# Kernel tuning notes

Measured on AMD Instinct MI355X. Metric: run time of the kernel, lower is better.

Reference implementation:

```python
import jax, jax.numpy as jnp
import numpy as np
import math

HID = 4096
SLOTS = 8
HEADS = 8
BD = 512  # bottleneck_dim
HD = BD // HEADS  # effective head dim = 64
B, S = 4, 4096


def setup_inputs() -> dict:
    key = jax.random.key(0)
    ks = jax.random.split(key, 8)
    std = 1.0 / math.sqrt(HID)
    return {
        "hidden_states": jax.random.normal(ks[0], (B, S, HID), dtype=jnp.float32),
        "attention_mask": jax.random.randint(ks[1], (B, S), 0, 2, dtype=jnp.int32),
        "memory_slots": jax.random.normal(ks[2], (SLOTS, HID), dtype=jnp.float32) * std,
        # torch nn.Linear weights are [out_features, in_features]
        "Wq": jax.random.normal(ks[3], (BD, HID), dtype=jnp.float32) * std,
        "Wk": jax.random.normal(ks[4], (BD, HID), dtype=jnp.float32) * std,
        "Wv": jax.random.normal(ks[5], (BD, HID), dtype=jnp.float32) * std,
        "Wo": jax.random.normal(ks[6], (HID, BD), dtype=jnp.float32) * (1.0 / math.sqrt(BD)),
    }


def reference(hidden_states, attention_mask, memory_slots, Wq, Wk, Wv, Wo):
    # Q from learnable slots (same for every batch element): [slots, BD]
    Q = memory_slots @ Wq.T
    Q = Q.reshape(SLOTS, HEADS, HD)                      # n h d
    # K/V from sequence: [b, s, BD] -> [b, s, h, d]
    K = jnp.einsum('bsi,oi->bso', hidden_states, Wk).reshape(B, S, HEADS, HD)
    V = jnp.einsum('bsi,oi->bso', hidden_states, Wv).reshape(B, S, HEADS, HD)
    # scores: [b, h, n, s]
    scores = jnp.einsum('nhd,bshd->bhns', Q, K) / jnp.sqrt(jnp.array(HD, scores_dtype := jnp.float32))
    mask = attention_mask[:, None, None, :]              # [b,1,1,s]
    scores = jnp.where(mask == 0, jnp.finfo(scores.dtype).min, scores)
    attn = jax.nn.softmax(scores, axis=-1)
    # output: [b, n, h, d] -> [b, n, BD]
    out = jnp.einsum('bhns,bshd->bnhd', attn, V).reshape(B, SLOTS, BD)
    # o_proj back to hidden_size
    return jnp.einsum('bnd,od->bno', out, Wo)            # [b, slots, HID]
```

## Files before the change

### kernel.cpp

```cpp
#include <hip/hip_runtime.h>
#include <math.h>

#define HID   4096
#define SLOTS 8
#define HEADS 8
#define BD    512
#define HD    64
#define BB    4
#define SS    4096
#define R64   64

typedef __attribute__((ext_vector_type(8))) short bf16x8;
typedef __attribute__((ext_vector_type(4))) float f32x4;

__device__ __forceinline__ unsigned short f2bf(float x) {
  unsigned int u = __builtin_bit_cast(unsigned int, x);
  return (unsigned short)((u + 0x7fffu + ((u >> 16) & 1u)) >> 16);
}


__global__ void q_kernel(const float* __restrict__ ms, const float* __restrict__ Wq,
                         float* __restrict__ Q) {
  int w = (blockIdx.x * blockDim.x + threadIdx.x) >> 6;
  int lane = threadIdx.x & 63;
  if (w >= SLOTS * BD) return;
  int n = w >> 9, o = w & (BD - 1);
  const float* a = ms + n * HID;
  const float* b = Wq + (size_t)o * HID;
  float acc = 0.f;
  for (int i = lane; i < HID; i += 64) acc = fmaf(a[i], b[i], acc);
  #pragma unroll
  for (int off = 32; off; off >>= 1) acc += __shfl_down(acc, off, 64);
  if (lane == 0) Q[w] = acc;
}

__global__ void qw_kernel(const float* __restrict__ Q, const float* __restrict__ Wk,
                          unsigned short* __restrict__ QW) {
  int idx = blockIdx.x * blockDim.x + threadIdx.x;
  int r = idx >> 12, i = idx & (HID - 1);
  int h = r >> 3, n = r & 7;
  const float* q  = Q + n * BD + h * HD;
  const float* wk = Wk + (size_t)(h * HD) * HID + i;
  float acc = 0.f;
  #pragma unroll 8
  for (int d = 0; d < HD; ++d) acc = fmaf(q[d], wk[(size_t)d * HID], acc);
  QW[idx] = f2bf(acc * 0.125f);
}

__global__ __launch_bounds__(256, 4) void scores_mfma(const float* __restrict__ hs,
                                                      const unsigned short* __restrict__ QW,
                                                      float* __restrict__ sp,
                                                      unsigned short* __restrict__ hsbf) {
  __shared__ unsigned short As[64 * 64];
  __shared__ unsigned short Bs[64 * 64];
  const int stile = blockIdx.x, ks = blockIdx.y, b = blockIdx.z;
  const int tid = threadIdx.x;
  const int wv = tid >> 6, lane = tid & 63;
  const int quad = lane >> 4, l16 = lane & 15;
  const int srow = tid >> 2, kc = (tid & 3) << 4;
  const int ch0 = (tid & 3) << 1;
  const int sw = srow & 7;
  const size_t arowoff = (size_t)(b * SS + stile * 64 + srow) * HID + ks * 1024 + kc;
  const float* hsp = hs + arowoff;
  unsigned short* hso = hsbf + arowoff;
  const unsigned short* qwp = QW + (size_t)srow * HID + ks * 1024 + kc;
  unsigned short* asw0 = &As[srow * 64 + (((ch0 + 0) ^ sw) << 3)];
  unsigned short* asw1 = &As[srow * 64 + (((ch0 + 1) ^ sw) << 3)];
  unsigned short* bsw0 = &Bs[srow * 64 + (((ch0 + 0) ^ sw) << 3)];
  unsigned short* bsw1 = &Bs[srow * 64 + (((ch0 + 1) ^ sw) << 3)];

  f32x4 acc[4] = {};
  float4 fa0 = *(const float4*)(hsp + 0);
  float4 fa1 = *(const float4*)(hsp + 4);
  float4 fa2 = *(const float4*)(hsp + 8);
  float4 fa3 = *(const float4*)(hsp + 12);
  uint4 qb0 = *(const uint4*)(qwp);
  uint4 qb1 = *(const uint4*)(qwp + 8);

  for (int c = 0; c < 16; ++c) {
    __syncthreads();
    union { unsigned short us[16]; uint4 q[2]; } u;
    float f[16] = {fa0.x, fa0.y, fa0.z, fa0.w, fa1.x, fa1.y, fa1.z, fa1.w,
                   fa2.x, fa2.y, fa2.z, fa2.w, fa3.x, fa3.y, fa3.z, fa3.w};
    #pragma unroll
    for (int j = 0; j < 16; ++j) u.us[j] = f2bf(f[j]);
    *(uint4*)asw0 = u.q[0];
    *(uint4*)asw1 = u.q[1];
    *(uint4*)bsw0 = qb0;
    *(uint4*)bsw1 = qb1;
    *(uint4*)(hso + (size_t)c * 64)     = u.q[0];
    *(uint4*)(hso + (size_t)c * 64 + 8) = u.q[1];
    __syncthreads();
    if (c < 15) {
      const float* p = hsp + (size_t)(c + 1) * 64;
      fa0 = *(const float4*)(p + 0);
      fa1 = *(const float4*)(p + 4);
      fa2 = *(const float4*)(p + 8);
      fa3 = *(const float4*)(p + 12);
      const unsigned short* q = qwp + (size_t)(c + 1) * 64;
      qb0 = *(const uint4*)(q);
      qb1 = *(const uint4*)(q + 8);
    }
    #pragma unroll
    for (int kk = 0; kk < 2; ++kk) {
      const int nrow = wv * 16 + l16;
      bf16x8 bfrag = *(const bf16x8*)&Bs[nrow * 64 + (((kk * 4 + quad) ^ (nrow & 7)) << 3)];
      #pragma unroll
      for (int mt = 0; mt < 4; ++mt) {
        const int mrow = mt * 16 + l16;
        bf16x8 afrag = *(const bf16x8*)&As[mrow * 64 + (((kk * 4 + quad) ^ (mrow & 7)) << 3)];
        acc[mt] = __builtin_amdgcn_mfma_f32_16x16x32_bf16(afrag, bfrag, acc[mt], 0, 0, 0);
      }
    }
  }
  const int r = wv * 16 + l16;
  #pragma unroll
  for (int mt = 0; mt < 4; ++mt) {
    int s = stile * 64 + mt * 16 + quad * 4;
    float4 v = make_float4(acc[mt][0], acc[mt][1], acc[mt][2], acc[mt][3]);
    *(float4*)(sp + (((size_t)ks * BB + b) * R64 + r) * SS + s) = v;
  }
}

__global__ __launch_bounds__(256) void softmax_kernel(const float* __restrict__ sp,
                                                      const int* __restrict__ mask,
                                                      unsigned short* __restrict__ attn) {
  int br = blockIdx.x;
  int b = br >> 6;
  int tid = threadIdx.x;
  const int* mrow = mask + b * SS;
  const size_t kstride = (size_t)BB * R64 * SS;
  float vals[16];
  float mx = -INFINITY;
  #pragma unroll
  for (int j = 0; j < 16; ++j) {
    int s = tid + j * 256;
    size_t o = (size_t)br * SS + s;
    float v = sp[o] + sp[o + kstride] + sp[o + 2 * kstride] + sp[o + 3 * kstride];
    if (mrow[s] == 0) v = -INFINITY;
    vals[j] = v;
    mx = fmaxf(mx, v);
  }
  __shared__ float redm[4], reds[4];
  #pragma unroll
  for (int off = 32; off; off >>= 1) mx = fmaxf(mx, __shfl_down(mx, off, 64));
  if ((tid & 63) == 0) redm[tid >> 6] = mx;
  __syncthreads();
  mx = fmaxf(fmaxf(redm[0], redm[1]), fmaxf(redm[2], redm[3]));
  float sum = 0.f;
  #pragma unroll
  for (int j = 0; j < 16; ++j) { vals[j] = expf(vals[j] - mx); sum += vals[j]; }
  #pragma unroll
  for (int off = 32; off; off >>= 1) sum += __shfl_down(sum, off, 64);
  if ((tid & 63) == 0) reds[tid >> 6] = sum;
  __syncthreads();
  sum = reds[0] + reds[1] + reds[2] + reds[3];
  float inv = 1.f / sum;
  #pragma unroll
  for (int j = 0; j < 16; ++j)
    attn[(size_t)br * SS + tid + j * 256] = f2bf(vals[j] * inv);
}

__global__ __launch_bounds__(256, 4) void ctx_mfma(const unsigned short* __restrict__ attn,
                                                   const unsigned short* __restrict__ hsbf,
                                                   float* __restrict__ cp) {
  __shared__ unsigned short As[64 * 64];
  __shared__ unsigned short Bs[64 * 64];
  const int itile = blockIdx.x, ss = blockIdx.y, b = blockIdx.z;
  const int tid = threadIdx.x;
  const int wv = tid >> 6, lane = tid & 63;
  const int quad = lane >> 4, l16 = lane & 15;
  const int arow = tid >> 2, asc = (tid & 3) << 4;
  const int ch0 = (tid & 3) << 1, swa = arow & 7;
  const unsigned short* ap = attn + (size_t)(b * R64 + arow) * SS + ss * 1024 + asc;
  unsigned short* asw0 = &As[arow * 64 + (((ch0 + 0) ^ swa) << 3)];
  unsigned short* asw1 = &As[arow * 64 + (((ch0 + 1) ^ swa) << 3)];
  const int p = tid & 31, g = tid >> 5;
  const unsigned short* bp0 = hsbf + (size_t)(b * SS + ss * 1024 + 2 * p) * HID + itile * 64 + g * 8;
  const unsigned short* bp1 = bp0 + HID;

  f32x4 acc[4] = {};
  uint4 aa0 = *(const uint4*)(ap);
  uint4 aa1 = *(const uint4*)(ap + 8);
  uint4 hb0 = *(const uint4*)(bp0);
  uint4 hb1 = *(const uint4*)(bp1);

  for (int c = 0; c < 16; ++c) {
    __syncthreads();
    *(uint4*)asw0 = aa0;
    *(uint4*)asw1 = aa1;
    {
      unsigned int lo[4] = {hb0.x, hb0.y, hb0.z, hb0.w};
      unsigned int hi[4] = {hb1.x, hb1.y, hb1.z, hb1.w};
      #pragma unroll
      for (int t = 0; t < 4; ++t) {
        unsigned int d0 = (lo[t] & 0xffffu) | (hi[t] << 16);
        unsigned int d1 = (lo[t] >> 16) | (hi[t] & 0xffff0000u);
        int i0 = g * 8 + 2 * t, i1 = i0 + 1;
        ((unsigned int*)Bs)[i0 * 32 + (((p >> 2) ^ (i0 & 7)) << 2) + (p & 3)] = d0;
        ((unsigned int*)Bs)[i1 * 32 + (((p >> 2) ^ (i1 & 7)) << 2) + (p & 3)] = d1;
      }
    }
    __syncthreads();
    if (c < 15) {
      const unsigned short* an = ap + (size_t)(c + 1) * 64;
      aa0 = *(const uint4*)(an);
      aa1 = *(const uint4*)(an + 8);
      const unsigned short* bn0 = bp0 + (size_t)(c + 1) * 64 * HID;
      hb0 = *(const uint4*)(bn0);
      hb1 = *(const uint4*)(bn0 + HID);
    }
    #pragma unroll
    for (int kk = 0; kk < 2; ++kk) {
      const int nrow = wv * 16 + l16;
      bf16x8 bfrag = *(const bf16x8*)&Bs[nrow * 64 + (((kk * 4 + quad) ^ (nrow & 7)) << 3)];
      #pragma unroll
      for (int mt = 0; mt < 4; ++mt) {
        const int mrow = mt * 16 + l16;
        bf16x8 afrag = *(const bf16x8*)&As[mrow * 64 + (((kk * 4 + quad) ^ (mrow & 7)) << 3)];
        acc[mt] = __builtin_amdgcn_mfma_f32_16x16x32_bf16(afrag, bfrag, acc[mt], 0, 0, 0);
      }
    }
  }
  const int i = itile * 64 + wv * 16 + l16;
  #pragma unroll
  for (int mt = 0; mt < 4; ++mt) {
    int r0 = mt * 16 + quad * 4;
    #pragma unroll
    for (int j = 0; j < 4; ++j)
      cp[(((size_t)ss * BB + b) * R64 + r0 + j) * HID + i] = acc[mt][j];
  }
}

__global__ void out_kernel(const float* __restrict__ cp, const float* __restrict__ Wv,
                           float* __restrict__ out) {
  int w = (blockIdx.x * blockDim.x + threadIdx.x) >> 6;
  int lane = threadIdx.x & 63;
  if (w >= BB * SLOTS * BD) return;
  int b = w >> 12, n = (w >> 9) & 7, hd = w & 511, h = hd >> 6;
  const size_t sstride = (size_t)BB * R64 * HID;
  const float* c  = cp + ((size_t)b * R64 + h * 8 + n) * HID;
  const float* wv = Wv + (size_t)hd * HID;
  float acc = 0.f;
  for (int i = lane; i < HID; i += 64) {
    float s = c[i] + c[i + sstride] + c[i + 2 * sstride] + c[i + 3 * sstride];
    acc = fmaf(s, wv[i], acc);
  }
  #pragma unroll
  for (int off = 32; off; off >>= 1) acc += __shfl_down(acc, off, 64);
  if (lane == 0) out[w] = acc;
}

__global__ void final_kernel(const float* __restrict__ out, const float* __restrict__ Wo,
                             float* __restrict__ y) {
  int w = (blockIdx.x * blockDim.x + threadIdx.x) >> 6;
  int lane = threadIdx.x & 63;
  if (w >= BB * SLOTS * HID) return;
  int bn = w >> 12, o = w & 4095;
  const float* orow = out + bn * BD;
  const float* wo = Wo + (size_t)o * BD;
  float acc = 0.f;
  #pragma unroll
  for (int d = lane; d < BD; d += 64) acc = fmaf(orow[d], wo[d], acc);
  #pragma unroll
  for (int off = 32; off; off >>= 1) acc += __shfl_down(acc, off, 64);
  if (lane == 0) y[w] = acc;
}

extern "C" void kernel_launch(void* const* d_in, const int* in_sizes, int n_in,
                              void* d_out, int out_size, void* d_ws, size_t ws_size,
                              hipStream_t stream) {
  const float* hs   = (const float*)d_in[0];
  const int*   mask = (const int*)d_in[1];
  const float* ms   = (const float*)d_in[2];
  const float* Wq   = (const float*)d_in[3];
  const float* Wk   = (const float*)d_in[4];
  const float* Wv   = (const float*)d_in[5];
  const float* Wo   = (const float*)d_in[6];

  char* ws = (char*)d_ws;
  float*          Q    = (float*)ws;          ws += 4096 * 4;
  unsigned short* QW   = (unsigned short*)ws; ws += (size_t)R64 * HID * 2;
  float*          sp   = (float*)ws;          ws += (size_t)4 * BB * R64 * SS * 4;
  unsigned short* attn = (unsigned short*)ws; ws += (size_t)BB * R64 * SS * 2;
  float*          cp   = (float*)ws;          ws += (size_t)4 * BB * R64 * HID * 4;
  unsigned short* hsbf = (unsigned short*)ws; ws += (size_t)BB * SS * HID * 2;
  float*          out  = (float*)ws;

  q_kernel<<<dim3((SLOTS * BD * 64) / 256), 256, 0, stream>>>(ms, Wq, Q);
  qw_kernel<<<dim3((R64 * HID) / 256), 256, 0, stream>>>(Q, Wk, QW);
  scores_mfma<<<dim3(64, 4, 4), 256, 0, stream>>>(hs, QW, sp, hsbf);
  softmax_kernel<<<dim3(BB * R64), 256, 0, stream>>>(sp, mask, attn);
  ctx_mfma<<<dim3(64, 4, 4), 256, 0, stream>>>(attn, hsbf, cp);
  out_kernel<<<dim3(4096), 256, 0, stream>>>(cp, Wv, out);
  final_kernel<<<dim3(32768), 256, 0, stream>>>(out, Wo, (float*)d_out);
}
```

Measured before the change: 582.8 us.

## Split fp32-to-bf16 conversion into a separate kernel and stream hidden states directly

```diff
diff --git a/kernel.cpp b/kernel.cpp
--- a/kernel.cpp
+++ b/kernel.cpp
@@ -18,6 +18,19 @@
   return (unsigned short)((u + 0x7fffu + ((u >> 16) & 1u)) >> 16);
 }
 
+__global__ __launch_bounds__(256) void cvt_kernel(const float4* __restrict__ hs,
+                                                  uint2* __restrict__ hsbf) {
+  const int nthreads = gridDim.x * 256;
+  int idx = blockIdx.x * 256 + threadIdx.x;
+  const int total = BB * SS * HID / 4;
+  for (; idx < total; idx += nthreads) {
+    float4 v = hs[idx];
+    uint2 o;
+    o.x = (unsigned int)f2bf(v.x) | ((unsigned int)f2bf(v.y) << 16);
+    o.y = (unsigned int)f2bf(v.z) | ((unsigned int)f2bf(v.w) << 16);
+    hsbf[idx] = o;
+  }
+}
 
 __global__ void q_kernel(const float* __restrict__ ms, const float* __restrict__ Wq,
                          float* __restrict__ Q) {
@@ -47,79 +60,49 @@
   QW[idx] = f2bf(acc * 0.125f);
 }
 
-__global__ __launch_bounds__(256, 4) void scores_mfma(const float* __restrict__ hs,
+__global__ __launch_bounds__(256, 4) void scores_mfma(const unsigned short* __restrict__ hsbf,
                                                       const unsigned short* __restrict__ QW,
-                                                      float* __restrict__ sp,
-                                                      unsigned short* __restrict__ hsbf) {
-  __shared__ unsigned short As[64 * 64];
-  __shared__ unsigned short Bs[64 * 64];
+                                                      float* __restrict__ sp) {
+  __shared__ unsigned short Qs[64 * 256];
   const int stile = blockIdx.x, ks = blockIdx.y, b = blockIdx.z;
   const int tid = threadIdx.x;
   const int wv = tid >> 6, lane = tid & 63;
   const int quad = lane >> 4, l16 = lane & 15;
-  const int srow = tid >> 2, kc = (tid & 3) << 4;
-  const int ch0 = (tid & 3) << 1;
-  const int sw = srow & 7;
-  const size_t arowoff = (size_t)(b * SS + stile * 64 + srow) * HID + ks * 1024 + kc;
-  const float* hsp = hs + arowoff;
-  unsigned short* hso = hsbf + arowoff;
-  const unsigned short* qwp = QW + (size_t)srow * HID + ks * 1024 + kc;
-  unsigned short* asw0 = &As[srow * 64 + (((ch0 + 0) ^ sw) << 3)];
-  unsigned short* asw1 = &As[srow * 64 + (((ch0 + 1) ^ sw) << 3)];
-  unsigned short* bsw0 = &Bs[srow * 64 + (((ch0 + 0) ^ sw) << 3)];
-  unsigned short* bsw1 = &Bs[srow * 64 + (((ch0 + 1) ^ sw) << 3)];
+  const int srow = tid >> 2, scb = (tid & 3) * 8, ssw = srow & 7;
+  const unsigned short* qwp = QW + (size_t)srow * HID + ks * 1024 + scb * 8;
+  const int s = stile * 64 + wv * 16 + l16;
+  const unsigned short* bp = hsbf + ((size_t)b * SS + s) * HID + ks * 1024 + quad * 8;
 
   f32x4 acc[4] = {};
-  float4 fa0 = *(const float4*)(hsp + 0);
-  float4 fa1 = *(const float4*)(hsp + 4);
-  float4 fa2 = *(const float4*)(hsp + 8);
-  float4 fa3 = *(const float4*)(hsp + 12);
-  uint4 qb0 = *(const uint4*)(qwp);
-  uint4 qb1 = *(const uint4*)(qwp + 8);
-
-  for (int c = 0; c < 16; ++c) {
-    __syncthreads();
-    union { unsigned short us[16]; uint4 q[2]; } u;
-    float f[16] = {fa0.x, fa0.y, fa0.z, fa0.w, fa1.x, fa1.y, fa1.z, fa1.w,
-                   fa2.x, fa2.y, fa2.z, fa2.w, fa3.x, fa3.y, fa3.z, fa3.w};
-    #pragma unroll
-    for (int j = 0; j < 16; ++j) u.us[j] = f2bf(f[j]);
-    *(uint4*)asw0 = u.q[0];
-    *(uint4*)asw1 = u.q[1];
-    *(uint4*)bsw0 = qb0;
-    *(uint4*)bsw1 = qb1;
-    *(uint4*)(hso + (size_t)c * 64)     = u.q[0];
-    *(uint4*)(hso + (size_t)c * 64 + 8) = u.q[1];
-    __syncthreads();
-    if (c < 15) {
-      const float* p = hsp + (size_t)(c + 1) * 64;
-      fa0 = *(const float4*)(p + 0);
-      fa1 = *(const float4*)(p + 4);
-      fa2 = *(const float4*)(p + 8);
-      fa3 = *(const float4*)(p + 12);
-      const unsigned short* q = qwp + (size_t)(c + 1) * 64;
-      qb0 = *(const uint4*)(q);
-      qb1 = *(const uint4*)(q + 8);
-    }
-    #pragma unroll
-    for (int kk = 0; kk < 2; ++kk) {
-      const int nrow = wv * 16 + l16;
-      bf16x8 bfrag = *(const bf16x8*)&Bs[nrow * 64 + (((kk * 4 + quad) ^ (nrow & 7)) << 3)];
+  for (int ck = 0; ck < 4; ++ck) {
+    __syncthreads();
+    #pragma unroll
+    for (int j = 0; j < 8; ++j) {
+      uint4 v = *(const uint4*)(qwp + ck * 256 + j * 8);
+      *(uint4*)&Qs[srow * 256 + (((scb + j) ^ ssw) << 3)] = v;
+    }
+    __syncthreads();
+    uint4 bf[8];
+    #pragma unroll
+    for (int ksub = 0; ksub < 8; ++ksub)
+      bf[ksub] = *(const uint4*)(bp + ck * 256 + ksub * 32);
+    #pragma unroll
+    for (int ksub = 0; ksub < 8; ++ksub) {
+      bf16x8 bfrag = __builtin_bit_cast(bf16x8, bf[ksub]);
       #pragma unroll
       for (int mt = 0; mt < 4; ++mt) {
-        const int mrow = mt * 16 + l16;
-        bf16x8 afrag = *(const bf16x8*)&As[mrow * 64 + (((kk * 4 + quad) ^ (mrow & 7)) << 3)];
+        const int rr = mt * 16 + l16;
+        const int c = ksub * 4 + quad;
+        bf16x8 afrag = *(const bf16x8*)&Qs[rr * 256 + ((c ^ (rr & 7)) << 3)];
         acc[mt] = __builtin_amdgcn_mfma_f32_16x16x32_bf16(afrag, bfrag, acc[mt], 0, 0, 0);
       }
     }
   }
-  const int r = wv * 16 + l16;
-  #pragma unroll
-  for (int mt = 0; mt < 4; ++mt) {
-    int s = stile * 64 + mt * 16 + quad * 4;
-    float4 v = make_float4(acc[mt][0], acc[mt][1], acc[mt][2], acc[mt][3]);
-    *(float4*)(sp + (((size_t)ks * BB + b) * R64 + r) * SS + s) = v;
-  }
+  #pragma unroll
+  for (int mt = 0; mt < 4; ++mt)
+    #pragma unroll
+    for (int j = 0; j < 4; ++j)
+      sp[(((size_t)ks * BB + b) * R64 + mt * 16 + quad * 4 + j) * SS + s] = acc[mt][j];
 }
 
 __global__ __launch_bounds__(256) void softmax_kernel(const float* __restrict__ sp,
@@ -287,9 +270,10 @@
   unsigned short* hsbf = (unsigned short*)ws; ws += (size_t)BB * SS * HID * 2;
   float*          out  = (float*)ws;
 
+  cvt_kernel<<<dim3(4096), 256, 0, stream>>>((const float4*)hs, (uint2*)hsbf);
   q_kernel<<<dim3((SLOTS * BD * 64) / 256), 256, 0, stream>>>(ms, Wq, Q);
   qw_kernel<<<dim3((R64 * HID) / 256), 256, 0, stream>>>(Q, Wk, QW);
-  scores_mfma<<<dim3(64, 4, 4), 256, 0, stream>>>(hs, QW, sp, hsbf);
+  scores_mfma<<<dim3(64, 4, 4), 256, 0, stream>>>(hsbf, QW, sp);
   softmax_kernel<<<dim3(BB * R64), 256, 0, stream>>>(sp, mask, attn);
   ctx_mfma<<<dim3(64, 4, 4), 256, 0, stream>>>(attn, hsbf, cp);
   out_kernel<<<dim3(4096), 256, 0, stream>>>(cp, Wv, out);
```

New measurement: 590.0 us. No clear change (+1.2%).
